# Performance work log

Hardware: AMD Instinct MI355X
Metric: run time of the kernel (lower is better)

## Reference

```python
import jax, jax.numpy as jnp
import numpy as np

N = 20000
E = 320000
IN = 256
H = 4
C = 64
NEG_SLOPE = 0.2


def setup_inputs() -> dict:
    key = jax.random.key(0)
    ks = jax.random.split(key, 12)
    HC = H * C

    def w(k, shape, fan_in):
        return jax.random.normal(k, shape, dtype=jnp.float32) / np.sqrt(fan_in)

    x = jax.random.normal(ks[0], (N, IN), dtype=jnp.float32)
    edge_index = jax.random.randint(ks[1], (2, E), 0, N, dtype=jnp.int64)
    return {
        "x": x,
        "edge_index": edge_index,
        "Wl1": w(ks[2], (IN, HC), IN),
        "Wr1": w(ks[3], (IN, HC), IN),
        "att1": w(ks[4], (H, C), C),
        "b1": jnp.zeros((HC,), dtype=jnp.float32),
        "Wl2": w(ks[5], (HC, HC), HC),
        "Wr2": w(ks[6], (HC, HC), HC),
        "att2": w(ks[7], (H, C), C),
        "b2": jnp.zeros((HC,), dtype=jnp.float32),
        "Wfc": w(ks[8], (HC, 2), HC),
        "bfc": jnp.zeros((2,), dtype=jnp.float32),
    }


def _gatv2(x, src, dst, Wl, Wr, att, b):
    """GATv2Conv (concat=True, share_weights=False), inference (no dropout)."""
    n = x.shape[0]
    xl = (x @ Wl).reshape(n, H, C)  # source-side projection
    xr = (x @ Wr).reshape(n, H, C)  # target-side projection
    # per-edge GATv2 score: a^T LeakyReLU(xl_j + xr_i)
    e = jax.nn.leaky_relu(xl[src] + xr[dst], NEG_SLOPE)      # [E, H, C]
    score = jnp.einsum("ehc,hc->eh", e, att)                 # [E, H]
    # segment softmax over incoming edges of each target node
    smax = jax.ops.segment_max(score, dst, num_segments=n)   # [N, H]
    ex = jnp.exp(score - smax[dst])
    denom = jax.ops.segment_sum(ex, dst, num_segments=n)     # [N, H]
    alpha = ex / denom[dst]                                  # [E, H]
    # scatter-aggregate messages (source projections weighted by alpha)
    out = jax.ops.segment_sum(alpha[:, :, None] * xl[src], dst, num_segments=n)
    return out.reshape(n, H * C) + b


def reference(x, edge_index, Wl1, Wr1, att1, b1, Wl2, Wr2, att2, b2, Wfc, bfc):
    n = x.shape[0]
    # add_self_loops=True (PyG default)
    loop = jnp.arange(n, dtype=edge_index.dtype)
    src = jnp.concatenate([edge_index[0], loop])
    dst = jnp.concatenate([edge_index[1], loop])

    h = _gatv2(x, src, dst, Wl1, Wr1, att1, b1)
    h = jax.nn.relu(h)
    h = _gatv2(h, src, dst, Wl2, Wr2, att2, b2)
    h = jax.nn.relu(h)
    g = jnp.mean(h, axis=0, keepdims=True)  # [1, H*C]
    return g @ Wfc + bfc                    # [1, 2]
```

## Files before the change

### kernel.cpp

```cpp
#include <hip/hip_runtime.h>
#include <hip/hip_bf16.h>
#include <math.h>

#define Nn 20000
#define Ee 320000
#define INF_ 256
#define Hh 4
#define Cc 64
#define HC 256
#define NEG_SLOPE 0.2f
#define NB 79

using frag16 = __attribute__((ext_vector_type(8))) short;
using f32x4  = __attribute__((ext_vector_type(4))) float;

__device__ __forceinline__ void async16(const void* g, void* l) {
    __builtin_amdgcn_global_load_lds(
        (const __attribute__((address_space(1))) unsigned int*)g,
        (__attribute__((address_space(3))) unsigned int*)l,
        16, 0, 0);
}


__global__ void init_deg(int* deg, int n) {
    int i = blockIdx.x * blockDim.x + threadIdx.x;
    if (i < n) deg[i] = 1;
}

__global__ void hist_kernel(const int* __restrict__ dst, int ne, int* deg) {
    int e = blockIdx.x * blockDim.x + threadIdx.x;
    if (e < ne) atomicAdd(&deg[dst[e]], 1);
}

__global__ __launch_bounds__(256) void scan1(const int* __restrict__ deg,
                                             int* __restrict__ excl,
                                             int* __restrict__ bsum, int n) {
    int tid = threadIdx.x;
    int gid = blockIdx.x * 256 + tid;
    int lane = tid & 63;
    int v = (gid < n) ? deg[gid] : 0;
    int x = v;
    #pragma unroll
    for (int off = 1; off < 64; off <<= 1) {
        int y = __shfl_up(x, off, 64);
        if (lane >= off) x += y;
    }
    __shared__ int wsum[4];
    if (lane == 63) wsum[tid >> 6] = x;
    __syncthreads();
    int wadd = 0;
    for (int w = 0; w < (tid >> 6); ++w) wadd += wsum[w];
    int incl = x + wadd;
    if (gid < n) excl[gid] = incl - v;
    if (tid == 255) bsum[blockIdx.x] = incl;
}

__global__ void scan2(const int* __restrict__ bsum, int* __restrict__ boff, int nb) {
    int lane = threadIdx.x;
    int carry = 0;
    for (int base = 0; base < nb; base += 64) {
        int i = base + lane;
        int v = (i < nb) ? bsum[i] : 0;
        int x = v;
        #pragma unroll
        for (int off = 1; off < 64; off <<= 1) {
            int y = __shfl_up(x, off, 64);
            if (lane >= off) x += y;
        }
        if (i < nb) boff[i] = carry + x - v;
        carry += __shfl(x, 63, 64);
    }
    if (lane == 0) boff[nb] = carry;
}

__global__ void scan_add(int* __restrict__ row_start, int* __restrict__ cursor,
                         const int* __restrict__ boff, int n, int nb) {
    int gid = blockIdx.x * blockDim.x + threadIdx.x;
    if (gid < n) {
        int v = row_start[gid] + boff[gid >> 8];
        row_start[gid] = v;
        cursor[gid] = v;
    }
    if (gid == n) row_start[n] = boff[nb];
}

__global__ void scatter_kernel(const int* __restrict__ src, const int* __restrict__ dst,
                               int ne, int n, int* cursor, int* colx) {
    int e = blockIdx.x * blockDim.x + threadIdx.x;
    if (e < ne) {
        int d = dst[e];
        int pos = atomicAdd(&cursor[d], 1);
        colx[pos] = src[e];
    } else if (e < ne + n) {
        int node = e - ne;
        int pos = atomicAdd(&cursor[node], 1);
        colx[pos] = node;
    }
}


__device__ inline unsigned short bf16rn(float f) {
    unsigned u = __float_as_uint(f);
    unsigned r = (u + 0x7FFFu + ((u >> 16) & 1u)) >> 16;
    return (unsigned short)r;
}

__device__ inline void split1(float v, short& h, short& l) {
    unsigned short hh = bf16rn(v);
    float back = __uint_as_float(((unsigned)hh) << 16);
    unsigned short ll = bf16rn(v - back);
    h = (short)hh; l = (short)ll;
}

__device__ __forceinline__ float4 bf4_to_f4(ushort4 u) {
    return make_float4(__uint_as_float((unsigned)u.x << 16),
                       __uint_as_float((unsigned)u.y << 16),
                       __uint_as_float((unsigned)u.z << 16),
                       __uint_as_float((unsigned)u.w << 16));
}


__global__ __launch_bounds__(256) void prep_kernel(const float* __restrict__ x,
                                                   const float* __restrict__ Wl1,
                                                   const float* __restrict__ Wr1,
                                                   const float* __restrict__ Wl2,
                                                   const float* __restrict__ Wr2,
                                                   short* __restrict__ WhT1,
                                                   short* __restrict__ WlT1,
                                                   short* __restrict__ WhT2,
                                                   short* __restrict__ WlT2,
                                                   short* __restrict__ Ah,
                                                   short* __restrict__ Al,
                                                   float* __restrict__ g,
                                                   int* __restrict__ fcnt, int n4) {
    int b = blockIdx.x;
    if (b < 1024) {
        int n = b & 255;
        int k = threadIdx.x;
        if (b == 0) {
            g[k] = 0.f;
            if (k == 0) *fcnt = 0;
        }
        const float* W = (b < 256) ? Wl1 : (b < 512) ? Wr1 : (b < 768) ? Wl2 : Wr2;
        short* Wh = (b < 512) ? WhT1 : WhT2;
        short* Wl = (b < 512) ? WlT1 : WlT2;
        int col = b & 511;
        float v = W[k * 256 + n];
        short h, l;
        split1(v, h, l);
        Wh[col * 256 + k] = h;
        Wl[col * 256 + k] = l;
    } else {
        int i = (b - 1024) * 256 + threadIdx.x;
        if (i >= n4) return;
        float4 v = ((const float4*)x)[i];
        short4 h, l;
        split1(v.x, h.x, l.x);
        split1(v.y, h.y, l.y);
        split1(v.z, h.z, l.z);
        split1(v.w, h.w, l.w);
        ((short4*)Ah)[i] = h;
        ((short4*)Al)[i] = l;
    }
}


#define BK 32

__global__ __launch_bounds__(256) void mfma_gemm(const short* __restrict__ Ah,
                                                 const short* __restrict__ Al,
                                                 const short* __restrict__ WhT,
                                                 const short* __restrict__ WlT,
                                                 unsigned short* __restrict__ XLh,
                                                 float* __restrict__ XR) {
    __shared__ short As_h[128 * BK];
    __shared__ short As_l[128 * BK];
    __shared__ short Bs_h[128 * BK];
    __shared__ short Bs_l[128 * BK];
    int tid = threadIdx.x;
    int wave = tid >> 6, lane = tid & 63;
    int quad = lane >> 4, lc = lane & 15;
    int bx = blockIdx.x;
    int bm = blockIdx.y * 128;
    int cbase = (bx * 128) & 255;

    int sr0 = wave * 32 + (lane >> 2);
    int sr1 = sr0 + 16;
    int koff = (lane & 3) * 8;
    int ga0 = bm + sr0; if (ga0 >= Nn) ga0 = Nn - 1;
    int ga1 = bm + sr1; if (ga1 >= Nn) ga1 = Nn - 1;
    int gb0 = bx * 128 + sr0;
    int gb1 = bx * 128 + sr1;
    int j0 = wave * 2, j1 = j0 + 1;

    f32x4 acc[2][8] = {};
    for (int c = 0; c < 8; ++c) {
        int k0 = c * BK;
        async16(Ah  + (size_t)ga0 * HC + k0 + koff, &As_h[j0 * 512]);
        async16(Ah  + (size_t)ga1 * HC + k0 + koff, &As_h[j1 * 512]);
        async16(Al  + (size_t)ga0 * HC + k0 + koff, &As_l[j0 * 512]);
        async16(Al  + (size_t)ga1 * HC + k0 + koff, &As_l[j1 * 512]);
        async16(WhT + (size_t)gb0 * HC + k0 + koff, &Bs_h[j0 * 512]);
        async16(WhT + (size_t)gb1 * HC + k0 + koff, &Bs_h[j1 * 512]);
        async16(WlT + (size_t)gb0 * HC + k0 + koff, &Bs_l[j0 * 512]);
        async16(WlT + (size_t)gb1 * HC + k0 + koff, &Bs_l[j1 * 512]);
        __syncthreads();

        frag16 a0h = *(const frag16*)&As_h[(wave * 32 + lc) * BK + quad * 8];
        frag16 a1h = *(const frag16*)&As_h[(wave * 32 + 16 + lc) * BK + quad * 8];
        frag16 a0l = *(const frag16*)&As_l[(wave * 32 + lc) * BK + quad * 8];
        frag16 a1l = *(const frag16*)&As_l[(wave * 32 + 16 + lc) * BK + quad * 8];
        #pragma unroll
        for (int t = 0; t < 8; ++t) {
            frag16 bh = *(const frag16*)&Bs_h[(t * 16 + lc) * BK + quad * 8];
            frag16 bl = *(const frag16*)&Bs_l[(t * 16 + lc) * BK + quad * 8];
            acc[0][t] = __builtin_amdgcn_mfma_f32_16x16x32_bf16(a0h, bh, acc[0][t], 0, 0, 0);
            acc[1][t] = __builtin_amdgcn_mfma_f32_16x16x32_bf16(a1h, bh, acc[1][t], 0, 0, 0);
            acc[0][t] = __builtin_amdgcn_mfma_f32_16x16x32_bf16(a0l, bh, acc[0][t], 0, 0, 0);
            acc[1][t] = __builtin_amdgcn_mfma_f32_16x16x32_bf16(a1l, bh, acc[1][t], 0, 0, 0);
            acc[0][t] = __builtin_amdgcn_mfma_f32_16x16x32_bf16(a0h, bl, acc[0][t], 0, 0, 0);
            acc[1][t] = __builtin_amdgcn_mfma_f32_16x16x32_bf16(a1h, bl, acc[1][t], 0, 0, 0);
        }
        __syncthreads();
    }
    #pragma unroll
    for (int mt = 0; mt < 2; ++mt) {
        int rbase = bm + wave * 32 + mt * 16 + quad * 4;
        #pragma unroll
        for (int t = 0; t < 8; ++t) {
            int col = cbase + t * 16 + lc;
            #pragma unroll
            for (int r = 0; r < 4; ++r) {
                int rw = rbase + r;
                if (rw >= Nn) continue;
                if (bx < 2) XLh[(size_t)rw * HC + col] = bf16rn(acc[mt][t][r]);
                else        XR [(size_t)rw * HC + col] = acc[mt][t][r];
            }
        }
    }
}


__device__ __forceinline__ float edge_score(const float4 v, const float4 xr,
                                            const float4 a06, const float4 a04) {
    float tx = v.x + xr.x, ty = v.y + xr.y, tz = v.z + xr.z, tw = v.w + xr.w;
    float p = a06.x * tx + a04.x * fabsf(tx);
    p += a06.y * ty + a04.y * fabsf(ty);
    p += a06.z * tz + a04.z * fabsf(tz);
    p += a06.w * tw + a04.w * fabsf(tw);
    p += __shfl_xor(p, 1, 64);
    p += __shfl_xor(p, 2, 64);
    p += __shfl_xor(p, 4, 64);
    p += __shfl_xor(p, 8, 64);
    return p;
}

__global__ __launch_bounds__(256) void gat_kernel(const ushort4* __restrict__ XL4,
                                                  const float4* __restrict__ XR4,
                                                  const int* __restrict__ row_start,
                                                  const int* __restrict__ colx,
                                                  const float4* __restrict__ att4,
                                                  const float4* __restrict__ bias4,
                                                  float4* __restrict__ Hout,
                                                  short4* __restrict__ Ahi,
                                                  short4* __restrict__ Alo,
                                                  int mode) {
    int wave = threadIdx.x >> 6, lane = threadIdx.x & 63;
    int node = blockIdx.x * 4 + wave;
    float4 xr = XR4[(size_t)node * 64 + lane];
    float4 a  = att4[lane];
    float4 a06 = make_float4(a.x * 0.6f, a.y * 0.6f, a.z * 0.6f, a.w * 0.6f);
    float4 a04 = make_float4(a.x * 0.4f, a.y * 0.4f, a.z * 0.4f, a.w * 0.4f);
    int e0 = row_start[node], e1 = row_start[node + 1];
    float l0 = 0.f, l1 = 0.f, l2 = 0.f, l3 = 0.f;
    float4 acc0 = make_float4(0.f, 0.f, 0.f, 0.f);
    float4 acc1 = make_float4(0.f, 0.f, 0.f, 0.f);
    float4 acc2 = make_float4(0.f, 0.f, 0.f, 0.f);
    float4 acc3 = make_float4(0.f, 0.f, 0.f, 0.f);
    int e = e0;
    for (; e + 3 < e1; e += 4) {
        int s0 = __builtin_amdgcn_readfirstlane(colx[e]);
        int s1 = __builtin_amdgcn_readfirstlane(colx[e + 1]);
        int s2 = __builtin_amdgcn_readfirstlane(colx[e + 2]);
        int s3 = __builtin_amdgcn_readfirstlane(colx[e + 3]);
        float4 v0 = bf4_to_f4(XL4[(size_t)s0 * 64 + lane]);
        float4 v1 = bf4_to_f4(XL4[(size_t)s1 * 64 + lane]);
        float4 v2 = bf4_to_f4(XL4[(size_t)s2 * 64 + lane]);
        float4 v3 = bf4_to_f4(XL4[(size_t)s3 * 64 + lane]);
        float pe0 = __expf(edge_score(v0, xr, a06, a04));
        float pe1 = __expf(edge_score(v1, xr, a06, a04));
        float pe2 = __expf(edge_score(v2, xr, a06, a04));
        float pe3 = __expf(edge_score(v3, xr, a06, a04));
        l0 += pe0; l1 += pe1; l2 += pe2; l3 += pe3;
        acc0.x += pe0 * v0.x; acc0.y += pe0 * v0.y; acc0.z += pe0 * v0.z; acc0.w += pe0 * v0.w;
        acc1.x += pe1 * v1.x; acc1.y += pe1 * v1.y; acc1.z += pe1 * v1.z; acc1.w += pe1 * v1.w;
        acc2.x += pe2 * v2.x; acc2.y += pe2 * v2.y; acc2.z += pe2 * v2.z; acc2.w += pe2 * v2.w;
        acc3.x += pe3 * v3.x; acc3.y += pe3 * v3.y; acc3.z += pe3 * v3.z; acc3.w += pe3 * v3.w;
    }
    for (; e < e1; ++e) {
        int s0 = __builtin_amdgcn_readfirstlane(colx[e]);
        float4 v0 = bf4_to_f4(XL4[(size_t)s0 * 64 + lane]);
        float pe0 = __expf(edge_score(v0, xr, a06, a04));
        l0 += pe0;
        acc0.x += pe0 * v0.x; acc0.y += pe0 * v0.y;
        acc0.z += pe0 * v0.z; acc0.w += pe0 * v0.w;
    }
    float rl = 1.f / (l0 + l1 + l2 + l3);
    float4 b = bias4[lane];
    float4 o = make_float4(fmaxf((acc0.x + acc1.x + acc2.x + acc3.x) * rl + b.x, 0.f),
                           fmaxf((acc0.y + acc1.y + acc2.y + acc3.y) * rl + b.y, 0.f),
                           fmaxf((acc0.z + acc1.z + acc2.z + acc3.z) * rl + b.z, 0.f),
                           fmaxf((acc0.w + acc1.w + acc2.w + acc3.w) * rl + b.w, 0.f));
    size_t oidx = (size_t)node * 64 + lane;
    if (mode) {
        short4 h4, l4;
        split1(o.x, h4.x, l4.x);
        split1(o.y, h4.y, l4.y);
        split1(o.z, h4.z, l4.z);
        split1(o.w, h4.w, l4.w);
        Ahi[oidx] = h4;
        Alo[oidx] = l4;
    } else {
        Hout[oidx] = o;
    }
}


__global__ __launch_bounds__(256) void colsum_fc(const float* __restrict__ Hmat,
                                                 float* __restrict__ g,
                                                 int* __restrict__ fcnt,
                                                 const float* __restrict__ Wfc,
                                                 const float* __restrict__ bfc,
                                                 float* __restrict__ out, float invN) {
    int ch = threadIdx.x;
    float s = 0.f;
    for (int r = blockIdx.x; r < Nn; r += gridDim.x)
        s += Hmat[(size_t)r * HC + ch];
    atomicAdd(&g[ch], s);
    __threadfence();
    __shared__ int last;
    if (ch == 0) last = (atomicAdd(fcnt, 1) == (int)gridDim.x - 1);
    __syncthreads();
    if (!last) return;
    float gv = atomicAdd(&g[ch], 0.f) * invN;
    float p0 = gv * Wfc[2 * ch];
    float p1 = gv * Wfc[2 * ch + 1];
    #pragma unroll
    for (int off = 32; off > 0; off >>= 1) {
        p0 += __shfl_xor(p0, off, 64);
        p1 += __shfl_xor(p1, off, 64);
    }
    __shared__ float s0[4], s1[4];
    if ((ch & 63) == 0) { s0[ch >> 6] = p0; s1[ch >> 6] = p1; }
    __syncthreads();
    if (ch == 0) {
        out[0] = s0[0] + s0[1] + s0[2] + s0[3] + bfc[0];
        out[1] = s1[0] + s1[1] + s1[2] + s1[3] + bfc[1];
    }
}


extern "C" void kernel_launch(void* const* d_in, const int* in_sizes, int n_in,
                              void* d_out, int out_size, void* d_ws, size_t ws_size,
                              hipStream_t stream) {
    const float* x    = (const float*)d_in[0];
    const int*   eidx = (const int*)d_in[1];
    const float* Wl1  = (const float*)d_in[2];
    const float* Wr1  = (const float*)d_in[3];
    const float* att1 = (const float*)d_in[4];
    const float* b1   = (const float*)d_in[5];
    const float* Wl2  = (const float*)d_in[6];
    const float* Wr2  = (const float*)d_in[7];
    const float* att2 = (const float*)d_in[8];
    const float* b2   = (const float*)d_in[9];
    const float* Wfc  = (const float*)d_in[10];
    const float* bfc  = (const float*)d_in[11];
    float* out = (float*)d_out;

    const int* srcv = eidx;
    const int* dstv = eidx + Ee;

    size_t NHC = (size_t)Nn * HC;
    float* XR = (float*)d_ws;
    float* Hb = XR + NHC;
    float* g  = Hb + NHC;
    unsigned short* XLh = (unsigned short*)(g + HC);
    short* Ah   = (short*)(XLh + NHC);
    short* Al   = Ah + NHC;
    short* WhT1 = Al + NHC;
    short* WlT1 = WhT1 + 512 * 256;
    short* WhT2 = WlT1 + 512 * 256;
    short* WlT2 = WhT2 + 512 * 256;
    int* deg       = (int*)(WlT2 + 512 * 256);
    int* row_start = deg + Nn;
    int* cursor    = row_start + (Nn + 1);
    int* colx      = cursor + Nn;
    int* bsum      = colx + (Ee + Nn);
    int* boff      = bsum + 128;
    int* fcnt      = boff + 128;

    const int N4 = (int)(NHC / 4);

    init_deg<<<(Nn + 255) / 256, 256, 0, stream>>>(deg, Nn);
    hist_kernel<<<(Ee + 255) / 256, 256, 0, stream>>>(dstv, Ee, deg);
    scan1<<<NB, 256, 0, stream>>>(deg, row_start, bsum, Nn);
    scan2<<<1, 64, 0, stream>>>(bsum, boff, NB);
    scan_add<<<(Nn + 256) / 256, 256, 0, stream>>>(row_start, cursor, boff, Nn, NB);
    scatter_kernel<<<(Ee + Nn + 255) / 256, 256, 0, stream>>>(srcv, dstv, Ee, Nn, cursor, colx);

    prep_kernel<<<1024 + N4 / 256, 256, 0, stream>>>(x, Wl1, Wr1, Wl2, Wr2,
                                                     WhT1, WlT1, WhT2, WlT2,
                                                     Ah, Al, g, fcnt, N4);

    dim3 ggrid(4, (Nn + 127) / 128);

    mfma_gemm<<<ggrid, 256, 0, stream>>>(Ah, Al, WhT1, WlT1, XLh, XR);
    gat_kernel<<<Nn / 4, 256, 0, stream>>>((const ushort4*)XLh, (const float4*)XR,
                                           row_start, colx, (const float4*)att1,
                                           (const float4*)b1, (float4*)Hb,
                                           (short4*)Ah, (short4*)Al, 1);

    mfma_gemm<<<ggrid, 256, 0, stream>>>(Ah, Al, WhT2, WlT2, XLh, XR);
    gat_kernel<<<Nn / 4, 256, 0, stream>>>((const ushort4*)XLh, (const float4*)XR,
                                           row_start, colx, (const float4*)att2,
                                           (const float4*)b2, (float4*)Hb,
                                           (short4*)Ah, (short4*)Al, 0);

    colsum_fc<<<256, 256, 0, stream>>>(Hb, g, fcnt, Wfc, bfc, out, 1.0f / Nn);
}
```

Measured before the change: 326.9 us.

## Double-buffer LDS tiles and XOR-swizzle k-chunks in the MFMA GEMM

```diff
diff --git a/kernel.cpp b/kernel.cpp
--- a/kernel.cpp
+++ b/kernel.cpp
@@ -173,10 +173,10 @@
                                                  const short* __restrict__ WlT,
                                                  unsigned short* __restrict__ XLh,
                                                  float* __restrict__ XR) {
-    __shared__ short As_h[128 * BK];
-    __shared__ short As_l[128 * BK];
-    __shared__ short Bs_h[128 * BK];
-    __shared__ short Bs_l[128 * BK];
+    __shared__ short As_h[2][128 * BK];
+    __shared__ short As_l[2][128 * BK];
+    __shared__ short Bs_h[2][128 * BK];
+    __shared__ short Bs_l[2][128 * BK];
     int tid = threadIdx.x;
     int wave = tid >> 6, lane = tid & 63;
     int quad = lane >> 4, lc = lane & 15;
@@ -186,34 +186,54 @@
 
     int sr0 = wave * 32 + (lane >> 2);
     int sr1 = sr0 + 16;
-    int koff = (lane & 3) * 8;
+    int swz = ((lane >> 2) ^ (lane >> 4)) & 3;
+    int koff = (((lane & 3) ^ swz)) * 8;
     int ga0 = bm + sr0; if (ga0 >= Nn) ga0 = Nn - 1;
     int ga1 = bm + sr1; if (ga1 >= Nn) ga1 = Nn - 1;
     int gb0 = bx * 128 + sr0;
     int gb1 = bx * 128 + sr1;
     int j0 = wave * 2, j1 = j0 + 1;
 
+    const short* pA0h = Ah  + (size_t)ga0 * HC + koff;
+    const short* pA1h = Ah  + (size_t)ga1 * HC + koff;
+    const short* pA0l = Al  + (size_t)ga0 * HC + koff;
+    const short* pA1l = Al  + (size_t)ga1 * HC + koff;
+    const short* pB0h = WhT + (size_t)gb0 * HC + koff;
+    const short* pB1h = WhT + (size_t)gb1 * HC + koff;
+    const short* pB0l = WlT + (size_t)gb0 * HC + koff;
+    const short* pB1l = WlT + (size_t)gb1 * HC + koff;
+
+    auto stage = [&](int c, int d) {
+        int k0 = c * BK;
+        async16(pA0h + k0, &As_h[d][j0 * 512]);
+        async16(pA1h + k0, &As_h[d][j1 * 512]);
+        async16(pA0l + k0, &As_l[d][j0 * 512]);
+        async16(pA1l + k0, &As_l[d][j1 * 512]);
+        async16(pB0h + k0, &Bs_h[d][j0 * 512]);
+        async16(pB1h + k0, &Bs_h[d][j1 * 512]);
+        async16(pB0l + k0, &Bs_l[d][j0 * 512]);
+        async16(pB1l + k0, &Bs_l[d][j1 * 512]);
+    };
+
+    int rs = (lc ^ (lc >> 2)) & 3;
+    int akb = ((quad ^ rs)) * 8;
+    int arow0 = (wave * 32 + lc) * BK + akb;
+    int arow1 = (wave * 32 + 16 + lc) * BK + akb;
+
     f32x4 acc[2][8] = {};
+    stage(0, 0);
     for (int c = 0; c < 8; ++c) {
-        int k0 = c * BK;
-        async16(Ah  + (size_t)ga0 * HC + k0 + koff, &As_h[j0 * 512]);
-        async16(Ah  + (size_t)ga1 * HC + k0 + koff, &As_h[j1 * 512]);
-        async16(Al  + (size_t)ga0 * HC + k0 + koff, &As_l[j0 * 512]);
-        async16(Al  + (size_t)ga1 * HC + k0 + koff, &As_l[j1 * 512]);
-        async16(WhT + (size_t)gb0 * HC + k0 + koff, &Bs_h[j0 * 512]);
-        async16(WhT + (size_t)gb1 * HC + k0 + koff, &Bs_h[j1 * 512]);
-        async16(WlT + (size_t)gb0 * HC + k0 + koff, &Bs_l[j0 * 512]);
-        async16(WlT + (size_t)gb1 * HC + k0 + koff, &Bs_l[j1 * 512]);
         __syncthreads();
-
-        frag16 a0h = *(const frag16*)&As_h[(wave * 32 + lc) * BK + quad * 8];
-        frag16 a1h = *(const frag16*)&As_h[(wave * 32 + 16 + lc) * BK + quad * 8];
-        frag16 a0l = *(const frag16*)&As_l[(wave * 32 + lc) * BK + quad * 8];
-        frag16 a1l = *(const frag16*)&As_l[(wave * 32 + 16 + lc) * BK + quad * 8];
+        if (c < 7) stage(c + 1, (c + 1) & 1);
+        int d = c & 1;
+        frag16 a0h = *(const frag16*)&As_h[d][arow0];
+        frag16 a1h = *(const frag16*)&As_h[d][arow1];
+        frag16 a0l = *(const frag16*)&As_l[d][arow0];
+        frag16 a1l = *(const frag16*)&As_l[d][arow1];
         #pragma unroll
         for (int t = 0; t < 8; ++t) {
-            frag16 bh = *(const frag16*)&Bs_h[(t * 16 + lc) * BK + quad * 8];
-            frag16 bl = *(const frag16*)&Bs_l[(t * 16 + lc) * BK + quad * 8];
+            frag16 bh = *(const frag16*)&Bs_h[d][(t * 16 + lc) * BK + akb];
+            frag16 bl = *(const frag16*)&Bs_l[d][(t * 16 + lc) * BK + akb];
             acc[0][t] = __builtin_amdgcn_mfma_f32_16x16x32_bf16(a0h, bh, acc[0][t], 0, 0, 0);
             acc[1][t] = __builtin_amdgcn_mfma_f32_16x16x32_bf16(a1h, bh, acc[1][t], 0, 0, 0);
             acc[0][t] = __builtin_amdgcn_mfma_f32_16x16x32_bf16(a0l, bh, acc[0][t], 0, 0, 0);
@@ -221,7 +241,6 @@
             acc[0][t] = __builtin_amdgcn_mfma_f32_16x16x32_bf16(a0h, bl, acc[0][t], 0, 0, 0);
             acc[1][t] = __builtin_amdgcn_mfma_f32_16x16x32_bf16(a1h, bl, acc[1][t], 0, 0, 0);
         }
-        __syncthreads();
     }
     #pragma unroll
     for (int mt = 0; mt < 2; ++mt) {
```

Result: no change. 330.4 us (+1.1%).

## Restructure MFMA GEMM with 64x64 tiles, double-buffered LDS, swizzle, XCD-aware mapping

Applied to the files above, without the earlier changes.

```diff
diff --git a/kernel.cpp b/kernel.cpp
--- a/kernel.cpp
+++ b/kernel.cpp
@@ -173,69 +173,71 @@
                                                  const short* __restrict__ WlT,
                                                  unsigned short* __restrict__ XLh,
                                                  float* __restrict__ XR) {
-    __shared__ short As_h[128 * BK];
-    __shared__ short As_l[128 * BK];
-    __shared__ short Bs_h[128 * BK];
-    __shared__ short Bs_l[128 * BK];
+    __shared__ short S[2][4][64 * BK];
     int tid = threadIdx.x;
     int wave = tid >> 6, lane = tid & 63;
     int quad = lane >> 4, lc = lane & 15;
-    int bx = blockIdx.x;
-    int bm = blockIdx.y * 128;
-    int cbase = (bx * 128) & 255;
-
-    int sr0 = wave * 32 + (lane >> 2);
-    int sr1 = sr0 + 16;
-    int koff = (lane & 3) * 8;
-    int ga0 = bm + sr0; if (ga0 >= Nn) ga0 = Nn - 1;
-    int ga1 = bm + sr1; if (ga1 >= Nn) ga1 = Nn - 1;
-    int gb0 = bx * 128 + sr0;
-    int gb1 = bx * 128 + sr1;
-    int j0 = wave * 2, j1 = j0 + 1;
-
-    f32x4 acc[2][8] = {};
+
+    int flat = blockIdx.x;
+    int xcd = flat & 7;
+    int slot = flat >> 3;
+    int rb = xcd + 8 * (slot >> 3);
+    int bxc = slot & 7;
+    int bm = rb * 64;
+    if (bm >= Nn) return;
+    int cbase = (bxc * 64) & 255;
+
+    int srow = lane >> 2;
+    int swz = ((lane >> 2) ^ (lane >> 4)) & 3;
+    int koff = ((lane & 3) ^ swz) * 8;
+    const short* mat = (wave == 0) ? Ah : (wave == 1) ? Al
+                     : (wave == 2) ? WhT : WlT;
+    int grow_base = (wave < 2) ? bm : bxc * 64;
+    const short* gp[4];
+    #pragma unroll
+    for (int i = 0; i < 4; ++i) {
+        int grow = grow_base + i * 16 + srow;
+        if (wave < 2 && grow >= Nn) grow = Nn - 1;
+        gp[i] = mat + (size_t)grow * HC + koff;
+    }
+
+    auto stage = [&](int c, int d) {
+        int k0 = c * BK;
+        #pragma unroll
+        for (int i = 0; i < 4; ++i)
+            async16(gp[i] + k0, &S[d][wave][i * 512]);
+    };
+
+    int rs = (lc ^ (lc >> 2)) & 3;
+    int akb = (quad ^ rs) * 8;
+
+    f32x4 acc[4] = {};
+    stage(0, 0);
     for (int c = 0; c < 8; ++c) {
-        int k0 = c * BK;
-        async16(Ah  + (size_t)ga0 * HC + k0 + koff, &As_h[j0 * 512]);
-        async16(Ah  + (size_t)ga1 * HC + k0 + koff, &As_h[j1 * 512]);
-        async16(Al  + (size_t)ga0 * HC + k0 + koff, &As_l[j0 * 512]);
-        async16(Al  + (size_t)ga1 * HC + k0 + koff, &As_l[j1 * 512]);
-        async16(WhT + (size_t)gb0 * HC + k0 + koff, &Bs_h[j0 * 512]);
-        async16(WhT + (size_t)gb1 * HC + k0 + koff, &Bs_h[j1 * 512]);
-        async16(WlT + (size_t)gb0 * HC + k0 + koff, &Bs_l[j0 * 512]);
-        async16(WlT + (size_t)gb1 * HC + k0 + koff, &Bs_l[j1 * 512]);
         __syncthreads();
-
-        frag16 a0h = *(const frag16*)&As_h[(wave * 32 + lc) * BK + quad * 8];
-        frag16 a1h = *(const frag16*)&As_h[(wave * 32 + 16 + lc) * BK + quad * 8];
-        frag16 a0l = *(const frag16*)&As_l[(wave * 32 + lc) * BK + quad * 8];
-        frag16 a1l = *(const frag16*)&As_l[(wave * 32 + 16 + lc) * BK + quad * 8];
-        #pragma unroll
-        for (int t = 0; t < 8; ++t) {
-            frag16 bh = *(const frag16*)&Bs_h[(t * 16 + lc) * BK + quad * 8];
-            frag16 bl = *(const frag16*)&Bs_l[(t * 16 + lc) * BK + quad * 8];
-            acc[0][t] = __builtin_amdgcn_mfma_f32_16x16x32_bf16(a0h, bh, acc[0][t], 0, 0, 0);
-            acc[1][t] = __builtin_amdgcn_mfma_f32_16x16x32_bf16(a1h, bh, acc[1][t], 0, 0, 0);
-            acc[0][t] = __builtin_amdgcn_mfma_f32_16x16x32_bf16(a0l, bh, acc[0][t], 0, 0, 0);
-            acc[1][t] = __builtin_amdgcn_mfma_f32_16x16x32_bf16(a1l, bh, acc[1][t], 0, 0, 0);
-            acc[0][t] = __builtin_amdgcn_mfma_f32_16x16x32_bf16(a0h, bl, acc[0][t], 0, 0, 0);
-            acc[1][t] = __builtin_amdgcn_mfma_f32_16x16x32_bf16(a1h, bl, acc[1][t], 0, 0, 0);
-        }
-        __syncthreads();
-    }
+        if (c < 7) stage(c + 1, (c + 1) & 1);
+        int d = c & 1;
+        frag16 bh = *(const frag16*)&S[d][2][(wave * 16 + lc) * BK + akb];
+        frag16 bl = *(const frag16*)&S[d][3][(wave * 16 + lc) * BK + akb];
+        #pragma unroll
+        for (int mt = 0; mt < 4; ++mt) {
+            frag16 amh = *(const frag16*)&S[d][0][(mt * 16 + lc) * BK + akb];
+            frag16 aml = *(const frag16*)&S[d][1][(mt * 16 + lc) * BK + akb];
+            acc[mt] = __builtin_amdgcn_mfma_f32_16x16x32_bf16(amh, bh, acc[mt], 0, 0, 0);
+            acc[mt] = __builtin_amdgcn_mfma_f32_16x16x32_bf16(aml, bh, acc[mt], 0, 0, 0);
+            acc[mt] = __builtin_amdgcn_mfma_f32_16x16x32_bf16(amh, bl, acc[mt], 0, 0, 0);
+        }
+    }
+    int col = cbase + wave * 16 + lc;
     #pragma unroll
-    for (int mt = 0; mt < 2; ++mt) {
-        int rbase = bm + wave * 32 + mt * 16 + quad * 4;
-        #pragma unroll
-        for (int t = 0; t < 8; ++t) {
-            int col = cbase + t * 16 + lc;
-            #pragma unroll
-            for (int r = 0; r < 4; ++r) {
-                int rw = rbase + r;
-                if (rw >= Nn) continue;
-                if (bx < 2) XLh[(size_t)rw * HC + col] = bf16rn(acc[mt][t][r]);
-                else        XR [(size_t)rw * HC + col] = acc[mt][t][r];
-            }
+    for (int mt = 0; mt < 4; ++mt) {
+        int rbase = bm + mt * 16 + quad * 4;
+        #pragma unroll
+        for (int r = 0; r < 4; ++r) {
+            int rw = rbase + r;
+            if (rw >= Nn) continue;
+            if (bxc < 4) XLh[(size_t)rw * HC + col] = bf16rn(acc[mt][r]);
+            else         XR [(size_t)rw * HC + col] = acc[mt][r];
         }
     }
 }
@@ -272,45 +274,61 @@
     float4 a06 = make_float4(a.x * 0.6f, a.y * 0.6f, a.z * 0.6f, a.w * 0.6f);
     float4 a04 = make_float4(a.x * 0.4f, a.y * 0.4f, a.z * 0.4f, a.w * 0.4f);
     int e0 = row_start[node], e1 = row_start[node + 1];
-    float l0 = 0.f, l1 = 0.f, l2 = 0.f, l3 = 0.f;
-    float4 acc0 = make_float4(0.f, 0.f, 0.f, 0.f);
-    float4 acc1 = make_float4(0.f, 0.f, 0.f, 0.f);
-    float4 acc2 = make_float4(0.f, 0.f, 0.f, 0.f);
-    float4 acc3 = make_float4(0.f, 0.f, 0.f, 0.f);
+    float lw[4] = {0.f, 0.f, 0.f, 0.f};
+    float4 acc[4];
+    #pragma unroll
+    for (int j = 0; j < 4; ++j) acc[j] = make_float4(0.f, 0.f, 0.f, 0.f);
+
     int e = e0;
+    for (; e + 7 < e1; e += 8) {
+        int s[8];
+        #pragma unroll
+        for (int j = 0; j < 8; ++j) s[j] = __builtin_amdgcn_readfirstlane(colx[e + j]);
+        float4 v[8];
+        #pragma unroll
+        for (int j = 0; j < 8; ++j) v[j] = bf4_to_f4(XL4[(size_t)s[j] * 64 + lane]);
+        #pragma unroll
+        for (int j = 0; j < 8; ++j) {
+            float pe = __expf(edge_score(v[j], xr, a06, a04));
+            lw[j & 3] += pe;
+            acc[j & 3].x += pe * v[j].x;
+            acc[j & 3].y += pe * v[j].y;
+            acc[j & 3].z += pe * v[j].z;
+            acc[j & 3].w += pe * v[j].w;
+        }
+    }
     for (; e + 3 < e1; e += 4) {
-        int s0 = __builtin_amdgcn_readfirstlane(colx[e]);
-        int s1 = __builtin_amdgcn_readfirstlane(colx[e + 1]);
-        int s2 = __builtin_amdgcn_readfirstlane(colx[e + 2]);
-        int s3 = __builtin_amdgcn_readfirstlane(colx[e + 3]);
-        float4 v0 = bf4_to_f4(XL4[(size_t)s0 * 64 + lane]);
-        float4 v1 = bf4_to_f4(XL4[(size_t)s1 * 64 + lane]);
-        float4 v2 = bf4_to_f4(XL4[(size_t)s2 * 64 + lane]);
-        float4 v3 = bf4_to_f4(XL4[(size_t)s3 * 64 + lane]);
-        float pe0 = __expf(edge_score(v0, xr, a06, a04));
-        float pe1 = __expf(edge_score(v1, xr, a06, a04));
-        float pe2 = __expf(edge_score(v2, xr, a06, a04));
-        float pe3 = __expf(edge_score(v3, xr, a06, a04));
-        l0 += pe0; l1 += pe1; l2 += pe2; l3 += pe3;
-        acc0.x += pe0 * v0.x; acc0.y += pe0 * v0.y; acc0.z += pe0 * v0.z; acc0.w += pe0 * v0.w;
-        acc1.x += pe1 * v1.x; acc1.y += pe1 * v1.y; acc1.z += pe1 * v1.z; acc1.w += pe1 * v1.w;
-        acc2.x += pe2 * v2.x; acc2.y += pe2 * v2.y; acc2.z += pe2 * v2.z; acc2.w += pe2 * v2.w;
-        acc3.x += pe3 * v3.x; acc3.y += pe3 * v3.y; acc3.z += pe3 * v3.z; acc3.w += pe3 * v3.w;
+        int s[4];
+        #pragma unroll
+        for (int j = 0; j < 4; ++j) s[j] = __builtin_amdgcn_readfirstlane(colx[e + j]);
+        float4 v[4];
+        #pragma unroll
+        for (int j = 0; j < 4; ++j) v[j] = bf4_to_f4(XL4[(size_t)s[j] * 64 + lane]);
+        #pragma unroll
+        for (int j = 0; j < 4; ++j) {
+            float pe = __expf(edge_score(v[j], xr, a06, a04));
+            lw[j] += pe;
+            acc[j].x += pe * v[j].x;
+            acc[j].y += pe * v[j].y;
+            acc[j].z += pe * v[j].z;
+            acc[j].w += pe * v[j].w;
+        }
     }
     for (; e < e1; ++e) {
         int s0 = __builtin_amdgcn_readfirstlane(colx[e]);
         float4 v0 = bf4_to_f4(XL4[(size_t)s0 * 64 + lane]);
-        float pe0 = __expf(edge_score(v0, xr, a06, a04));
-        l0 += pe0;
-        acc0.x += pe0 * v0.x; acc0.y += pe0 * v0.y;
-        acc0.z += pe0 * v0.z; acc0.w += pe0 * v0.w;
-    }
-    float rl = 1.f / (l0 + l1 + l2 + l3);
+        float pe = __expf(edge_score(v0, xr, a06, a04));
+        lw[0] += pe;
+        acc[0].x += pe * v0.x; acc[0].y += pe * v0.y;
+        acc[0].z += pe * v0.z; acc[0].w += pe * v0.w;
+    }
+    float rl = 1.f / (lw[0] + lw[1] + lw[2] + lw[3]);
     float4 b = bias4[lane];
-    float4 o = make_float4(fmaxf((acc0.x + acc1.x + acc2.x + acc3.x) * rl + b.x, 0.f),
-                           fmaxf((acc0.y + acc1.y + acc2.y + acc3.y) * rl + b.y, 0.f),
-                           fmaxf((acc0.z + acc1.z + acc2.z + acc3.z) * rl + b.z, 0.f),
-                           fmaxf((acc0.w + acc1.w + acc2.w + acc3.w) * rl + b.w, 0.f));
+    float4 o = make_float4(
+        fmaxf((acc[0].x + acc[1].x + acc[2].x + acc[3].x) * rl + b.x, 0.f),
+        fmaxf((acc[0].y + acc[1].y + acc[2].y + acc[3].y) * rl + b.y, 0.f),
+        fmaxf((acc[0].z + acc[1].z + acc[2].z + acc[3].z) * rl + b.z, 0.f),
+        fmaxf((acc[0].w + acc[1].w + acc[2].w + acc[3].w) * rl + b.w, 0.f));
     size_t oidx = (size_t)node * 64 + lane;
     if (mode) {
         short4 h4, l4;
@@ -412,15 +430,15 @@
                                                      WhT1, WlT1, WhT2, WlT2,
                                                      Ah, Al, g, fcnt, N4);
 
-    dim3 ggrid(4, (Nn + 127) / 128);
-
-    mfma_gemm<<<ggrid, 256, 0, stream>>>(Ah, Al, WhT1, WlT1, XLh, XR);
+    const int GEMM_BLOCKS = 320 * 8;
+
+    mfma_gemm<<<GEMM_BLOCKS, 256, 0, stream>>>(Ah, Al, WhT1, WlT1, XLh, XR);
     gat_kernel<<<Nn / 4, 256, 0, stream>>>((const ushort4*)XLh, (const float4*)XR,
                                            row_start, colx, (const float4*)att1,
                                            (const float4*)b1, (float4*)Hb,
                                            (short4*)Ah, (short4*)Al, 1);
 
-    mfma_gemm<<<ggrid, 256, 0, stream>>>(Ah, Al, WhT2, WlT2, XLh, XR);
+    mfma_gemm<<<GEMM_BLOCKS, 256, 0, stream>>>(Ah, Al, WhT2, WlT2, XLh, XR);
     gat_kernel<<<Nn / 4, 256, 0, stream>>>((const ushort4*)XLh, (const float4*)XR,
                                            row_start, colx, (const float4*)att2,
                                            (const float4*)b2, (float4*)Hb,
```

New measurement: 322.2 us. No clear change (-1.4%).
